# Optimization experiments

Hardware: AMD Instinct MI355X
Metric: run time of the kernel (lower is better)

The kernel has to match this reference:

```python
import jax, jax.numpy as jnp
import numpy as np

B, S, F, H, D = 32, 512, 32, 8, 300   # batch, seq, n_features, hidden_dim, n_dim_model
FH = min(D, F)                        # flattened GRN hidden = min(n_dim_model, n_features)


def _p(key, shape, scale=0.05):
    return (jax.random.normal(key, shape) * scale).astype(jnp.float32)


def setup_inputs() -> dict:
    key = jax.random.key(0)
    ks = jax.random.split(key, 16)
    return {
        "x": jax.random.normal(ks[0], (B, S, F), dtype=jnp.float32),
        "pre_w": _p(ks[1], (F, H)), "pre_b": _p(ks[2], (F, H)),
        "sg_fc1_w": _p(ks[3], (F, H, H)), "sg_fc1_b": _p(ks[4], (F, H)),
        "sg_fc2_w": _p(ks[5], (F, H, D)), "sg_fc2_b": _p(ks[6], (F, D)),
        "sg_gate_w": _p(ks[7], (F, D, 2 * D)), "sg_gate_b": _p(ks[8], (F, 2 * D)),
        "sg_ln_g": jnp.ones((F, D), jnp.float32), "sg_ln_b": jnp.zeros((F, D), jnp.float32),
        "fl_fc1_w": _p(ks[9], (F * H, FH)), "fl_fc1_b": _p(ks[10], (FH,)),
        "fl_fc2_w": _p(ks[11], (FH, F)), "fl_fc2_b": _p(ks[12], (F,)),
        "fl_gate_w": _p(ks[13], (F, 2 * F)), "fl_gate_b": _p(ks[14], (2 * F,)),
        "fl_ln_g": jnp.ones((F,), jnp.float32), "fl_ln_b": jnp.zeros((F,), jnp.float32),
    }


def _interp_last(x, out_dim):
    # torch F.interpolate(mode='linear', align_corners=True) along the last axis
    in_dim = x.shape[-1]
    pos = jnp.arange(out_dim) * ((in_dim - 1) / (out_dim - 1))
    lo = jnp.floor(pos).astype(jnp.int32)
    hi = jnp.minimum(lo + 1, in_dim - 1)
    w = (pos - lo.astype(pos.dtype)).astype(x.dtype)
    return x[..., lo] * (1 - w) + x[..., hi] * w


def _layer_norm(x, g, b, eps=1e-5):
    m = jnp.mean(x, axis=-1, keepdims=True)
    v = jnp.var(x, axis=-1, keepdims=True)
    return (x - m) * jax.lax.rsqrt(v + eps) * g + b


def _forward(x, pre_w, pre_b, sg_fc1_w, sg_fc1_b, sg_fc2_w, sg_fc2_b,
             sg_gate_w, sg_gate_b, sg_ln_g, sg_ln_b,
             fl_fc1_w, fl_fc1_b, fl_fc2_w, fl_fc2_b, fl_gate_w, fl_gate_b,
             fl_ln_g, fl_ln_b):
    # per-feature prescaler: Linear(1, H) for each of F features, batched
    pre = x[..., None] * pre_w + pre_b                                   # [B,S,F,H]

    # per-feature GRN (H -> H -> D), batched over the feature axis f
    h = jax.nn.elu(jnp.einsum('bsfh,fhk->bsfk', pre, sg_fc1_w) + sg_fc1_b)
    h = jnp.einsum('bsfk,fkd->bsfd', h, sg_fc2_w) + sg_fc2_b             # [B,S,F,D]
    g = jnp.einsum('bsfd,fdp->bsfp', h, sg_gate_w) + sg_gate_b           # [B,S,F,2D]
    glu = g[..., :D] * jax.nn.sigmoid(g[..., D:])
    residual = _interp_last(pre, D)                                      # H -> D interpolate projection
    outputs = _layer_norm(glu + residual, sg_ln_g, sg_ln_b)              # [B,S,F,D]

    # flattened GRN on concatenated prescaler outputs (F*H -> FH -> F)
    flat = pre.reshape(pre.shape[0], pre.shape[1], F * H)                # matches torch.cat order
    fh = jax.nn.elu(flat @ fl_fc1_w + fl_fc1_b)
    fh = fh @ fl_fc2_w + fl_fc2_b                                        # [B,S,F]
    fg = fh @ fl_gate_w + fl_gate_b                                      # [B,S,2F]
    fglu = fg[..., :F] * jax.nn.sigmoid(fg[..., F:])
    wlogits = _layer_norm(fglu + _interp_last(flat, F), fl_ln_g, fl_ln_b)
    w = jax.nn.softmax(wlogits, axis=-1)                                 # [B,S,F]

    out = jnp.einsum('bsfd,bsf->bsd', outputs, w)                        # softmax-weighted sum over features
    return out, w[..., None, :]                                          # weights unsqueezed at dim -2


def reference(x, pre_w, pre_b, sg_fc1_w, sg_fc1_b, sg_fc2_w, sg_fc2_b,
              sg_gate_w, sg_gate_b, sg_ln_g, sg_ln_b,
              fl_fc1_w, fl_fc1_b, fl_fc2_w, fl_fc2_b, fl_gate_w, fl_gate_b,
              fl_ln_g, fl_ln_b):
    return _forward(x, pre_w, pre_b, sg_fc1_w, sg_fc1_b, sg_fc2_w, sg_fc2_b,
                    sg_gate_w, sg_gate_b, sg_ln_g, sg_ln_b,
                    fl_fc1_w, fl_fc1_b, fl_fc2_w, fl_fc2_b, fl_gate_w, fl_gate_b,
                    fl_ln_g, fl_ln_b)
```

## Files before the change

### kernel.cpp

```cpp
#include <hip/hip_runtime.h>
#include <hip/hip_bf16.h>

#define NB 32
#define NS 512
#define NF 32
#define NH 8
#define ND 300
#define NTOK (NB*NS)
#define TPW 4
#define WPB 4
#define TPB (TPW*WPB)

using bf16 = __hip_bfloat16;
typedef float v2f __attribute__((ext_vector_type(2)));

__device__ __forceinline__ float rcpf_(float x){ return __builtin_amdgcn_rcpf(x); }
__device__ __forceinline__ float rsqf_(float x){ return __builtin_amdgcn_rsqf(x); }
__device__ __forceinline__ float sigm(float x){ return rcpf_(1.0f + __expf(-x)); }
__device__ __forceinline__ float eluf(float x){ return x > 0.0f ? x : __expf(x) - 1.0f; }

__device__ __forceinline__ v2f fma2(v2f a, v2f b, v2f c){
    return __builtin_elementwise_fma(a, b, c);
}
__device__ __forceinline__ v2f fma2s(float s, v2f b, v2f c){
    return __builtin_elementwise_fma((v2f){s, s}, b, c);
}

template<int BF16>
__device__ __forceinline__ float ldf(const void* p, size_t i){
    if (BF16) return __bfloat162float(((const bf16*)p)[i]);
    return ((const float*)p)[i];
}
template<int BF16>
__device__ __forceinline__ void stf(void* p, size_t i, float v){
    if (BF16) ((bf16*)p)[i] = __float2bfloat16(v);
    else      ((float*)p)[i] = v;
}

__device__ __forceinline__ bool is_bf16(const void* ones){
    return *(const unsigned*)ones == 0x3F803F80u;
}

template<int CTRL>
__device__ __forceinline__ float dppadd(float v){
    return v + __int_as_float(__builtin_amdgcn_update_dpp(
        0, __float_as_int(v), CTRL, 0xF, 0xF, true));
}
template<int CTRL>
__device__ __forceinline__ float dppmax(float v){
    return fmaxf(v, __int_as_float(__builtin_amdgcn_update_dpp(
        __float_as_int(v), __float_as_int(v), CTRL, 0xF, 0xF, false)));
}
__device__ __forceinline__ float rlane(float v, int l){
    return __int_as_float(__builtin_amdgcn_readlane(__float_as_int(v), l));
}
__device__ __forceinline__ float wsum64(float v){
    v = dppadd<0x111>(v); v = dppadd<0x112>(v); v = dppadd<0x114>(v); v = dppadd<0x118>(v);
    v = dppadd<0x142>(v); v = dppadd<0x143>(v);
    return rlane(v, 63);
}
__device__ __forceinline__ float rsum32(float v){
    v = dppadd<0x111>(v); v = dppadd<0x112>(v); v = dppadd<0x114>(v); v = dppadd<0x118>(v);
    return rlane(v, 15) + rlane(v, 31);
}
__device__ __forceinline__ float rmax32(float v){
    v = dppmax<0x111>(v); v = dppmax<0x112>(v); v = dppmax<0x114>(v); v = dppmax<0x118>(v);
    return fmaxf(rlane(v, 15), rlane(v, 31));
}

template<int BF16>
__device__ void precompute_body(const void* __restrict__ W2, const void* __restrict__ b2,
                                const void* __restrict__ Wg, const void* __restrict__ bg,
                                const void* __restrict__ sg_g, const void* __restrict__ sg_b,
                                float* __restrict__ Crow, float (*part)[64][10])
{
    const int tid = threadIdx.x;
    const int l = tid & 63;
    const int q = tid >> 6;
    const int fj = blockIdx.x * 64 + l;
    const int f = fj / 600;
    const int j = fj % 600;

    const size_t WgBase = (size_t)f * 180000 + j;
    const size_t W2Base = (size_t)f * 2400;
    const size_t b2Base = (size_t)f * 300;

    float acc[8] = {0,0,0,0,0,0,0,0};
    float accb = 0.f;
    for (int m = q * 75; m < q * 75 + 75; ++m) {
        float wg = ldf<BF16>(Wg, WgBase + (size_t)m * 600);
        #pragma unroll
        for (int k = 0; k < 8; ++k)
            acc[k] += ldf<BF16>(W2, W2Base + (size_t)k * 300 + m) * wg;
        accb += ldf<BF16>(b2, b2Base + m) * wg;
    }
    #pragma unroll
    for (int k = 0; k < 8; ++k) part[q][l][k] = acc[k];
    part[q][l][8] = accb;
    __syncthreads();

    const int d = (j < 300) ? j : j - 300;
    const int half = (j < 300) ? 0 : 1;
    float* row = Crow + ((size_t)f * 300 + d) * 20;
    for (int v = q; v < 9; v += 4) {
        float s = part[0][l][v] + part[1][l][v] + part[2][l][v] + part[3][l][v];
        if (v < 8) {
            row[2 * v + half] = s;
        } else {
            float bc = s + ldf<BF16>(bg, (size_t)f * 600 + j);
            if (j < 300) {
                row[16] = bc;
                row[18] = ldf<BF16>(sg_g, (size_t)f * 300 + d);
                row[19] = ldf<BF16>(sg_b, (size_t)f * 300 + d);
            } else {
                row[17] = bc;
            }
        }
    }
}

__global__ void precompute_kernel(const void* __restrict__ W2, const void* __restrict__ b2,
                                  const void* __restrict__ Wg, const void* __restrict__ bg,
                                  const void* __restrict__ sg_g, const void* __restrict__ sg_b,
                                  float* __restrict__ Crow)
{
    __shared__ float part[4][64][10];
    if (is_bf16(sg_g))
        precompute_body<1>(W2, b2, Wg, bg, sg_g, sg_b, Crow, part);
    else
        precompute_body<0>(W2, b2, Wg, bg, sg_g, sg_b, Crow, part);
}

template<int BF16>
__device__ void vsn_body(const void* __restrict__ x,
                         const void* __restrict__ pre_w, const void* __restrict__ pre_b,
                         const void* __restrict__ W1,    const void* __restrict__ b1,
                         const void* __restrict__ fl1w,  const void* __restrict__ fl1b,
                         const void* __restrict__ fl2w,  const void* __restrict__ fl2b,
                         const void* __restrict__ flgw,  const void* __restrict__ flgb,
                         const void* __restrict__ flng,  const void* __restrict__ flnb,
                         const float* __restrict__ Crow,
                         void* __restrict__ d_out, float* preS_, float* hS_)
{
    void* outMain = d_out;
    void* outW    = (char*)d_out + (size_t)NTOK * ND * (BF16 ? 2 : 4);

    const int tid  = threadIdx.x;
    const int wave = tid >> 6;
    const int lane = tid & 63;
    const int tokBase = blockIdx.x * TPB + wave * TPW;

    float* myPre = preS_ + wave * (TPW * 256);
    float* myH   = hS_   + wave * (TPW * 256);

    {
        float pw[4], pb[4];
        #pragma unroll
        for (int q = 0; q < 4; ++q) {
            pw[q] = ldf<BF16>(pre_w, 4 * lane + q);
            pb[q] = ldf<BF16>(pre_b, 4 * lane + q);
        }
        const int fidx = lane >> 1;
        #pragma unroll
        for (int t = 0; t < TPW; ++t) {
            float xv = ldf<BF16>(x, (size_t)(tokBase + t) * NF + fidx);
            float4 v;
            v.x = xv * pw[0] + pb[0];
            v.y = xv * pw[1] + pb[1];
            v.z = xv * pw[2] + pb[2];
            v.w = xv * pw[3] + pb[3];
            *(float4*)(&myPre[t * 256 + 4 * lane]) = v;
        }
    }

    {
        const int f  = lane >> 1;
        const int kh = (lane & 1) * 4;
        float w1r[8][4], b1r[4];
        #pragma unroll
        for (int m = 0; m < 8; ++m)
            #pragma unroll
            for (int q = 0; q < 4; ++q)
                w1r[m][q] = ldf<BF16>(W1, (size_t)(f * 8 + m) * 8 + kh + q);
        #pragma unroll
        for (int q = 0; q < 4; ++q) b1r[q] = ldf<BF16>(b1, f * 8 + kh + q);

        #pragma unroll
        for (int t = 0; t < TPW; ++t) {
            float pr[8];
            float4 pA = *(const float4*)(&myPre[t * 256 + f * 8]);
            float4 pB = *(const float4*)(&myPre[t * 256 + f * 8 + 4]);
            pr[0]=pA.x; pr[1]=pA.y; pr[2]=pA.z; pr[3]=pA.w;
            pr[4]=pB.x; pr[5]=pB.y; pr[6]=pB.z; pr[7]=pB.w;
            float a[4] = {b1r[0], b1r[1], b1r[2], b1r[3]};
            #pragma unroll
            for (int m = 0; m < 8; ++m)
                #pragma unroll
                for (int q = 0; q < 4; ++q)
                    a[q] += pr[m] * w1r[m][q];
            float4 hv4;
            hv4.x = eluf(a[0]); hv4.y = eluf(a[1]); hv4.z = eluf(a[2]); hv4.w = eluf(a[3]);
            *(float4*)(&myH[t * 256 + 4 * lane]) = hv4;
        }
    }

    const int jj = lane & 31;
    const int hB = lane >> 5;
    float wreg[TPW];
    {
        float f1b = (hB == 0) ? ldf<BF16>(fl1b, jj) : 0.0f;
        v2f p1a = {f1b, f1b};
        v2f p1b = {f1b, f1b};
        for (int k = 0; k < 128; ++k) {
            int kk = hB * 128 + k;
            float wv = ldf<BF16>(fl1w, (size_t)kk * 32 + jj);
            v2f wvv = {wv, wv};
            p1a = fma2((v2f){myPre[0 * 256 + kk], myPre[1 * 256 + kk]}, wvv, p1a);
            p1b = fma2((v2f){myPre[2 * 256 + kk], myPre[3 * 256 + kk]}, wvv, p1b);
        }
        float p1[TPW] = {p1a.x, p1a.y, p1b.x, p1b.y};
        float fhv[TPW];
        #pragma unroll
        for (int t = 0; t < TPW; ++t)
            fhv[t] = eluf(p1[t] + __shfl_xor(p1[t], 32));

        float p2[TPW];
        float f2b = ldf<BF16>(fl2b, jj);
        #pragma unroll
        for (int t = 0; t < TPW; ++t) p2[t] = f2b;
        #pragma unroll
        for (int k = 0; k < 32; ++k) {
            float wv = ldf<BF16>(fl2w, k * 32 + jj);
            #pragma unroll
            for (int t = 0; t < TPW; ++t) p2[t] += rlane(fhv[t], k) * wv;
        }
        float p3[TPW];
        float fgbv = ldf<BF16>(flgb, lane);
        #pragma unroll
        for (int t = 0; t < TPW; ++t) p3[t] = fgbv;
        #pragma unroll
        for (int k = 0; k < 32; ++k) {
            float wv = ldf<BF16>(flgw, k * 64 + lane);
            #pragma unroll
            for (int t = 0; t < TPW; ++t) p3[t] += rlane(p2[t], k) * wv;
        }

        float lng = ldf<BF16>(flng, jj), lnb = ldf<BF16>(flnb, jj);
        float posB = (float)jj * (255.0f / 31.0f);
        int loB = (int)floorf(posB); loB = loB < 0 ? 0 : (loB > 254 ? 254 : loB);
        float frB = posB - (float)loB;

        #pragma unroll
        for (int t = 0; t < TPW; ++t) {
            float fgA  = __shfl(p3[t], jj);
            float fgB  = __shfl(p3[t], jj + 32);
            float fglu = fgA * sigm(fgB);
            float pl = myPre[t * 256 + loB];
            float ph = myPre[t * 256 + loB + 1];
            float tv = fglu + pl + frB * (ph - pl);
            float S1 = rsum32(tv);
            float S2 = rsum32(tv * tv);
            float mean = S1 * (1.0f / 32.0f);
            float var  = fmaxf(S2 * (1.0f / 32.0f) - mean * mean, 0.0f);
            float rs   = rsqf_(var + 1e-5f);
            float wl   = (tv - mean) * rs * lng + lnb;
            float mx   = rmax32(wl);
            float e    = __expf(wl - mx);
            float ss   = rsum32(e);
            float wv   = e * rcpf_(ss);
            wreg[t] = wv;
            if (lane < 32) stf<BF16>(outW, (size_t)(tokBase + t) * NF + lane, wv);
        }
    }

    int lo_[5]; float fr_[5];
    #pragma unroll
    for (int i = 0; i < 5; ++i) {
        int d = i * 64 + lane;
        float pos = (float)d * (7.0f / 299.0f);
        int lo = (int)floorf(pos); lo = lo < 0 ? 0 : (lo > 6 ? 6 : lo);
        lo_[i] = lo; fr_[i] = pos - (float)lo;
    }

    float acc[TPW][5];
    #pragma unroll
    for (int t = 0; t < TPW; ++t)
        #pragma unroll
        for (int i = 0; i < 5; ++i) acc[t][i] = 0.0f;

    for (int f = 0; f < NF; ++f) {
        float hv[TPW][8];
        #pragma unroll
        for (int t = 0; t < TPW; ++t) {
            float4 h0 = *(const float4*)(&myH[t * 256 + f * 8]);
            float4 h1 = *(const float4*)(&myH[t * 256 + f * 8 + 4]);
            hv[t][0]=h0.x; hv[t][1]=h0.y; hv[t][2]=h0.z; hv[t][3]=h0.w;
            hv[t][4]=h1.x; hv[t][5]=h1.y; hv[t][6]=h1.z; hv[t][7]=h1.w;
        }

        float tt[TPW][5], s1[TPW], s2[TPW], lgv[5], lbv[5];
        #pragma unroll
        for (int t = 0; t < TPW; ++t) { s1[t] = 0.0f; s2[t] = 0.0f; }

        #pragma unroll
        for (int i = 0; i < 5; ++i) {
            int d = i * 64 + lane;
            bool ok = (d < ND);
            const float4* row = (const float4*)(Crow + ((size_t)f * ND + (ok ? d : ND - 1)) * 20);
            float4 q0 = row[0], q1 = row[1], q2 = row[2], q3 = row[3], ex = row[4];
            v2f P0 = {q0.x, q0.y}, P1 = {q0.z, q0.w};
            v2f P2 = {q1.x, q1.y}, P3 = {q1.z, q1.w};
            v2f P4 = {q2.x, q2.y}, P5 = {q2.z, q2.w};
            v2f P6 = {q3.x, q3.y}, P7 = {q3.z, q3.w};
            lgv[i] = ex.z; lbv[i] = ex.w;
            int base = f * 8 + lo_[i];
            #pragma unroll
            for (int t = 0; t < TPW; ++t) {
                const float* h = hv[t];
                v2f g = {ex.x, ex.y};
                g = fma2s(h[0], P0, g);
                g = fma2s(h[1], P1, g);
                g = fma2s(h[2], P2, g);
                g = fma2s(h[3], P3, g);
                g = fma2s(h[4], P4, g);
                g = fma2s(h[5], P5, g);
                g = fma2s(h[6], P6, g);
                g = fma2s(h[7], P7, g);
                float pl = myPre[t * 256 + base];
                float ph = myPre[t * 256 + base + 1];
                float tv = g.x * sigm(g.y) + pl + fr_[i] * (ph - pl);
                tv = ok ? tv : 0.0f;
                tt[t][i] = tv; s1[t] += tv; s2[t] += tv * tv;
            }
        }

        #pragma unroll
        for (int t = 0; t < TPW; ++t) {
            float S1 = wsum64(s1[t]);
            float S2 = wsum64(s2[t]);
            float mean = S1 * (1.0f / 300.0f);
            float var  = fmaxf(S2 * (1.0f / 300.0f) - mean * mean, 0.0f);
            float rs   = rsqf_(var + 1e-5f);
            float wf   = rlane(wreg[t], f);
            float wrs  = wf * rs;
            #pragma unroll
            for (int i = 0; i < 5; ++i) {
                int d = i * 64 + lane;
                if (d < ND) {
                    float a = wrs * lgv[i];
                    acc[t][i] += a * tt[t][i] + (wf * lbv[i] - a * mean);
                }
            }
        }
    }

    #pragma unroll
    for (int t = 0; t < TPW; ++t) {
        const size_t tok = (size_t)tokBase + t;
        #pragma unroll
        for (int i = 0; i < 5; ++i) {
            int d = i * 64 + lane;
            if (d < ND) stf<BF16>(outMain, tok * ND + d, acc[t][i]);
        }
    }
}

__launch_bounds__(256, 2)
__global__ void vsn_main(const void* __restrict__ x,
                         const void* __restrict__ pre_w, const void* __restrict__ pre_b,
                         const void* __restrict__ W1,    const void* __restrict__ b1,
                         const void* __restrict__ fl1w,  const void* __restrict__ fl1b,
                         const void* __restrict__ fl2w,  const void* __restrict__ fl2b,
                         const void* __restrict__ flgw,  const void* __restrict__ flgb,
                         const void* __restrict__ flng,  const void* __restrict__ flnb,
                         const float* __restrict__ Crow, void* __restrict__ d_out)
{
    __shared__ float preS_[WPB * TPW * 256];
    __shared__ float hS_[WPB * TPW * 256];
    if (is_bf16(flng))
        vsn_body<1>(x, pre_w, pre_b, W1, b1, fl1w, fl1b, fl2w, fl2b,
                    flgw, flgb, flng, flnb, Crow, d_out, preS_, hS_);
    else
        vsn_body<0>(x, pre_w, pre_b, W1, b1, fl1w, fl1b, fl2w, fl2b,
                    flgw, flgb, flng, flnb, Crow, d_out, preS_, hS_);
}

extern "C" void kernel_launch(void* const* d_in, const int* in_sizes, int n_in,
                              void* d_out, int out_size, void* d_ws, size_t ws_size,
                              hipStream_t stream)
{
    const void* x     = d_in[0];
    const void* pre_w = d_in[1];
    const void* pre_b = d_in[2];
    const void* W1    = d_in[3];
    const void* b1    = d_in[4];
    const void* W2    = d_in[5];
    const void* b2    = d_in[6];
    const void* Wg    = d_in[7];
    const void* bg    = d_in[8];
    const void* sg_g  = d_in[9];
    const void* sg_b  = d_in[10];
    const void* fl1w  = d_in[11];
    const void* fl1b  = d_in[12];
    const void* fl2w  = d_in[13];
    const void* fl2b  = d_in[14];
    const void* flgw  = d_in[15];
    const void* flgb  = d_in[16];
    const void* flng  = d_in[17];
    const void* flnb  = d_in[18];

    float* Crow = (float*)d_ws;

    precompute_kernel<<<300, 256, 0, stream>>>(W2, b2, Wg, bg, sg_g, sg_b, Crow);

    vsn_main<<<NTOK / TPB, 256, 0, stream>>>(x, pre_w, pre_b, W1, b1,
        fl1w, fl1b, fl2w, fl2b, flgw, flgb, flng, flnb, Crow, d_out);
}
```

Baseline: 334.1 us.

## Stage W2/b2 in LDS for precompute, vectorize fl1 LDS reads, relax launch bounds

The precompute kernel now cooperatively loads the per-feature W2 and b2 slices into shared memory (up to two features per block), so the inner loop stops re-reading global memory. In the main kernel, the flattened fc1 loop reads the prescaled activations as float4 from LDS, processing four k values per iteration. The launch bounds drop the min-blocks-per-SM hint, which lets the compiler use more registers but may lower occupancy. Together these mix LDS staging, vectorized loads and a register/occupancy trade-off.

```diff
diff --git a/kernel.cpp b/kernel.cpp
--- a/kernel.cpp
+++ b/kernel.cpp
@@ -72,7 +72,8 @@
 __device__ void precompute_body(const void* __restrict__ W2, const void* __restrict__ b2,
                                 const void* __restrict__ Wg, const void* __restrict__ bg,
                                 const void* __restrict__ sg_g, const void* __restrict__ sg_b,
-                                float* __restrict__ Crow, float (*part)[64][10])
+                                float* __restrict__ Crow,
+                                float (*part)[64][10], float (*w2s)[2400], float (*b2s)[300])
 {
     const int tid = threadIdx.x;
     const int l = tid & 63;
@@ -81,9 +82,20 @@
     const int f = fj / 600;
     const int j = fj % 600;
 
+    const int fLo = (blockIdx.x * 64) / 600;
+    const int fHi = (blockIdx.x * 64 + 63) / 600;
+
+    for (int ff = 0; ff <= fHi - fLo; ++ff) {
+        for (int idx = tid; idx < 2400; idx += 256)
+            w2s[ff][idx] = ldf<BF16>(W2, (size_t)(fLo + ff) * 2400 + idx);
+        for (int idx = tid; idx < 300; idx += 256)
+            b2s[ff][idx] = ldf<BF16>(b2, (size_t)(fLo + ff) * 300 + idx);
+    }
+    __syncthreads();
+
+    const float* myW2 = w2s[f - fLo];
+    const float* myB2 = b2s[f - fLo];
     const size_t WgBase = (size_t)f * 180000 + j;
-    const size_t W2Base = (size_t)f * 2400;
-    const size_t b2Base = (size_t)f * 300;
 
     float acc[8] = {0,0,0,0,0,0,0,0};
     float accb = 0.f;
@@ -91,8 +103,8 @@
         float wg = ldf<BF16>(Wg, WgBase + (size_t)m * 600);
         #pragma unroll
         for (int k = 0; k < 8; ++k)
-            acc[k] += ldf<BF16>(W2, W2Base + (size_t)k * 300 + m) * wg;
-        accb += ldf<BF16>(b2, b2Base + m) * wg;
+            acc[k] += myW2[k * 300 + m] * wg;
+        accb += myB2[m] * wg;
     }
     #pragma unroll
     for (int k = 0; k < 8; ++k) part[q][l][k] = acc[k];
@@ -125,10 +137,12 @@
                                   float* __restrict__ Crow)
 {
     __shared__ float part[4][64][10];
+    __shared__ float w2s[2][2400];
+    __shared__ float b2s[2][300];
     if (is_bf16(sg_g))
-        precompute_body<1>(W2, b2, Wg, bg, sg_g, sg_b, Crow, part);
+        precompute_body<1>(W2, b2, Wg, bg, sg_g, sg_b, Crow, part, w2s, b2s);
     else
-        precompute_body<0>(W2, b2, Wg, bg, sg_g, sg_b, Crow, part);
+        precompute_body<0>(W2, b2, Wg, bg, sg_g, sg_b, Crow, part, w2s, b2s);
 }
 
 template<int BF16>
@@ -210,15 +224,27 @@
     {
         float f1b = (hB == 0) ? ldf<BF16>(fl1b, jj) : 0.0f;
         v2f p1a = {f1b, f1b};
-        v2f p1b = {f1b, f1b};
-        for (int k = 0; k < 128; ++k) {
-            int kk = hB * 128 + k;
-            float wv = ldf<BF16>(fl1w, (size_t)kk * 32 + jj);
-            v2f wvv = {wv, wv};
-            p1a = fma2((v2f){myPre[0 * 256 + kk], myPre[1 * 256 + kk]}, wvv, p1a);
-            p1b = fma2((v2f){myPre[2 * 256 + kk], myPre[3 * 256 + kk]}, wvv, p1b);
-        }
-        float p1[TPW] = {p1a.x, p1a.y, p1b.x, p1b.y};
+        v2f p1c = {f1b, f1b};
+        for (int kg = 0; kg < 32; ++kg) {
+            const int kk = hB * 128 + kg * 4;
+            float4 pr0 = *(const float4*)(&myPre[0 * 256 + kk]);
+            float4 pr1 = *(const float4*)(&myPre[1 * 256 + kk]);
+            float4 pr2 = *(const float4*)(&myPre[2 * 256 + kk]);
+            float4 pr3 = *(const float4*)(&myPre[3 * 256 + kk]);
+            float w0 = ldf<BF16>(fl1w, (size_t)(kk + 0) * 32 + jj);
+            float w1 = ldf<BF16>(fl1w, (size_t)(kk + 1) * 32 + jj);
+            float w2 = ldf<BF16>(fl1w, (size_t)(kk + 2) * 32 + jj);
+            float w3 = ldf<BF16>(fl1w, (size_t)(kk + 3) * 32 + jj);
+            p1a = fma2((v2f){pr0.x, pr1.x}, (v2f){w0, w0}, p1a);
+            p1c = fma2((v2f){pr2.x, pr3.x}, (v2f){w0, w0}, p1c);
+            p1a = fma2((v2f){pr0.y, pr1.y}, (v2f){w1, w1}, p1a);
+            p1c = fma2((v2f){pr2.y, pr3.y}, (v2f){w1, w1}, p1c);
+            p1a = fma2((v2f){pr0.z, pr1.z}, (v2f){w2, w2}, p1a);
+            p1c = fma2((v2f){pr2.z, pr3.z}, (v2f){w2, w2}, p1c);
+            p1a = fma2((v2f){pr0.w, pr1.w}, (v2f){w3, w3}, p1a);
+            p1c = fma2((v2f){pr2.w, pr3.w}, (v2f){w3, w3}, p1c);
+        }
+        float p1[TPW] = {p1a.x, p1a.y, p1c.x, p1c.y};
         float fhv[TPW];
         #pragma unroll
         for (int t = 0; t < TPW; ++t)
@@ -365,7 +391,7 @@
     }
 }
 
-__launch_bounds__(256, 2)
+__launch_bounds__(256)
 __global__ void vsn_main(const void* __restrict__ x,
                          const void* __restrict__ pre_w, const void* __restrict__ pre_b,
                          const void* __restrict__ W1,    const void* __restrict__ b1,
```

Measured after the change: 328.5 us. About the same (-1.7%).
